# Optimization experiments

Hardware: AMD Instinct MI355X
Metric: run time of the kernel (lower is better)

Reference implementation:

```python
import jax, jax.numpy as jnp
import numpy as np

DIM = 384
NUM_HEADS = 12
WIN = (8, 8, 8)
Q_TOK = 1
K_TOK = 1
B = 64
N = WIN[0] * WIN[1] * WIN[2]  # 512


def _build_rel_index():
    t = max(Q_TOK, K_TOK)
    max_rel = [(w - 1) * t for w in WIN]
    nbins = [2 * m + 1 for m in max_rel]
    def coords(tok):
        axes = [np.arange(WIN[i]) * tok for i in range(3)]
        g = np.stack(np.meshgrid(*axes, indexing='ij'))  # [3, D, H, W]
        return g.reshape(3, -1)  # [3, N]
    cq = coords(Q_TOK)
    ck = coords(K_TOK)
    rel = (cq[:, :, None] - ck[:, None, :]).transpose(1, 2, 0)  # [N, N, 3]
    rel = rel + np.array(max_rel)
    idx = rel[..., 0] * (nbins[1] * nbins[2]) + rel[..., 1] * nbins[2] + rel[..., 2]
    return idx.astype(np.int32), nbins[0] * nbins[1] * nbins[2]


def setup_inputs() -> dict:
    key = jax.random.key(0)
    ks = jax.random.split(key, 7)
    rel_index_np, num_rel = _build_rel_index()
    s = 0.02
    return {
        'x1': jax.random.normal(ks[0], (B, N, DIM), jnp.float32),
        'x2': jax.random.normal(ks[1], (B, N, DIM), jnp.float32),
        'Wq': jax.random.normal(ks[2], (DIM, DIM), jnp.float32) * s,
        'Wkv': jax.random.normal(ks[3], (2 * DIM, DIM), jnp.float32) * s,
        'q_bias': jax.random.normal(ks[4], (DIM,), jnp.float32) * s,
        'v_bias': jax.random.normal(ks[5], (DIM,), jnp.float32) * s,
        'bias_table': jax.random.normal(ks[6], (num_rel, NUM_HEADS), jnp.float32) * s,
        'rel_index': jnp.asarray(rel_index_np),  # [N, N] int32
    }


def reference(x1, x2, Wq, Wkv, q_bias, v_bias, bias_table, rel_index):
    Bq, N1, C = x1.shape
    N2 = x2.shape[1]
    H = NUM_HEADS
    hd = C // H

    q = x1 @ Wq.T + q_bias                      # [B, N1, C]
    kv_bias = jnp.concatenate([jnp.zeros_like(v_bias), v_bias])
    kv = x2 @ Wkv.T + kv_bias                   # [B, N2, 2C]

    q = q.reshape(Bq, N1, H, hd).transpose(0, 2, 1, 3)   # [B, H, N1, hd]
    kv = kv.reshape(Bq, N2, 2, H, hd).transpose(2, 0, 3, 1, 4)
    k, v = kv[0], kv[1]                          # [B, H, N2, hd]

    # relative position bias: gather [N1, N2, H] -> [H, N1, N2]
    bias = bias_table[rel_index]                 # [N1, N2, H]
    bias = bias.transpose(2, 0, 1)               # [H, N1, N2]

    scale = 1.0 / jnp.sqrt(jnp.asarray(hd, q.dtype))
    scores = jnp.einsum('bhqd,bhkd->bhqk', q, k) * scale + bias[None]
    attn = jax.nn.softmax(scores, axis=-1)
    out = jnp.einsum('bhqk,bhkd->bhqd', attn, v)  # [B, H, N1, hd]
    return out.transpose(0, 2, 1, 3).reshape(Bq, N1, C)
```

## Files before the change

### kernel.cpp

```cpp
#include <hip/hip_runtime.h>

typedef unsigned short u16;
typedef unsigned int u32;
typedef __bf16 bf16x8 __attribute__((ext_vector_type(8)));
typedef float f32x4 __attribute__((ext_vector_type(4)));
typedef u16 u16x8 __attribute__((ext_vector_type(8)));
typedef u32 u32x4 __attribute__((ext_vector_type(4)));

#define NB 64
#define NN 512
#define NH 12
#define HD 32
#define DIM 384

static constexpr size_t QWS = (size_t)NB * NH * NN * HD;
#define LOG2E 1.4426950408889634f
#define QSCALE 0.25503486f

__device__ __forceinline__ u16 f2bf(float f) {
  __bf16 b = (__bf16)f;
  union { __bf16 b; u16 u; } v; v.b = b;
  return v.u;
}
__device__ __forceinline__ float lo16f(u32 w) {
  union { u32 u; float f; } v; v.u = w << 16;
  return v.f;
}
__device__ __forceinline__ float hi16f(u32 w) {
  union { u32 u; float f; } v; v.u = w & 0xffff0000u;
  return v.f;
}

__global__ __launch_bounds__(256) void bias_expand_k(const float* __restrict__ table,
                                                     const int* __restrict__ rel,
                                                     u32* __restrict__ beR) {
  int t = blockIdx.x * 256 + threadIdx.x;
  int word = t & 3;
  int lane = (t >> 2) & 63;
  int mf   = (t >> 8) & 3;
  int wv   = (t >> 10) & 7;
  int kt   = (t >> 13) & 15;
  int h    = t >> 17;
  int lr = lane & 15, lg = lane >> 4;
  int q = wv * 64 + mf * 16 + lr;
  int k = kt * 32 + (word >> 1) * 16 + lg * 4 + (word & 1) * 2;
  int i0 = rel[q * NN + k];
  int i1 = rel[q * NN + k + 1];
  u16 b0 = f2bf(table[i0 * NH + h] * LOG2E);
  u16 b1 = f2bf(table[i1 * NH + h] * LOG2E);
  beR[t] = (u32)b0 | ((u32)b1 << 16);
}

__global__ __launch_bounds__(256) void qkv_proj_k(const float* __restrict__ x1,
                                                  const float* __restrict__ x2,
                                                  const float* __restrict__ Wq,
                                                  const float* __restrict__ Wkv,
                                                  const float* __restrict__ qb,
                                                  const float* __restrict__ vb,
                                                  u16* __restrict__ q_ws,
                                                  u16* __restrict__ k_ws,
                                                  u16* __restrict__ v_ws) {
  const int g = blockIdx.x;
  const int v = (g & 7) * 288 + (g >> 3);
  const int ct = v % 9;
  const int m0 = (v / 9) * 128;
  const int j0 = ct * 128;
  const float* A;
  const float* W;
  int type;
  if (ct < 3)      { A = x1; W = Wq  + (size_t)j0 * DIM;         type = 0; }
  else if (ct < 6) { A = x2; W = Wkv + (size_t)(j0 - 384) * DIM; type = 1; }
  else             { A = x2; W = Wkv + (size_t)(j0 - 384) * DIM; type = 2; }

  __shared__ u16 As[128][72];
  __shared__ u16 Bs[128][72];

  const int tid = threadIdx.x;
  const int lane = tid & 63, wid = tid >> 6;
  const int wm = (wid >> 1) * 64, wn = (wid & 1) * 64;
  const int lg = lane >> 4, lr = lane & 15;
  const int srow = tid >> 3;
  const int scol = (tid & 7) * 8;

  f32x4 acc[4][4] = {};

  for (int k0 = 0; k0 < DIM; k0 += 64) {
    __syncthreads();
#pragma unroll
    for (int rr = 0; rr < 4; ++rr) {
      int r = srow + rr * 32;
      const float* src = A + (size_t)(m0 + r) * DIM + k0 + scol;
      float4 f0 = *(const float4*)src;
      float4 f1 = *(const float4*)(src + 4);
      u16x8 tmp = {f2bf(f0.x), f2bf(f0.y), f2bf(f0.z), f2bf(f0.w),
                   f2bf(f1.x), f2bf(f1.y), f2bf(f1.z), f2bf(f1.w)};
      *(u16x8*)&As[r][scol] = tmp;
      const float* srcB = W + (size_t)r * DIM + k0 + scol;
      float4 g0 = *(const float4*)srcB;
      float4 g1 = *(const float4*)(srcB + 4);
      u16x8 tmpB = {f2bf(g0.x), f2bf(g0.y), f2bf(g0.z), f2bf(g0.w),
                    f2bf(g1.x), f2bf(g1.y), f2bf(g1.z), f2bf(g1.w)};
      *(u16x8*)&Bs[r][scol] = tmpB;
    }
    __syncthreads();
#pragma unroll
    for (int kk = 0; kk < 2; ++kk) {
      bf16x8 af[4], bfv[4];
#pragma unroll
      for (int mf = 0; mf < 4; ++mf)
        af[mf] = *(const bf16x8*)&As[wm + mf * 16 + lr][kk * 32 + lg * 8];
#pragma unroll
      for (int nf = 0; nf < 4; ++nf)
        bfv[nf] = *(const bf16x8*)&Bs[wn + nf * 16 + lr][kk * 32 + lg * 8];
#pragma unroll
      for (int mf = 0; mf < 4; ++mf)
#pragma unroll
        for (int nf = 0; nf < 4; ++nf)
          acc[mf][nf] = __builtin_amdgcn_mfma_f32_16x16x32_bf16(af[mf], bfv[nf], acc[mf][nf], 0, 0, 0);
    }
  }

  const int b = m0 >> 9;
  u16* dst = (type == 0) ? q_ws : (type == 1 ? k_ws : v_ws);
  const float scale = (type == 0) ? QSCALE : 1.0f;
#pragma unroll
  for (int nf = 0; nf < 4; ++nf) {
    int j = j0 + wn + nf * 16 + lr;
    int jj = j - ((type == 0) ? 0 : (type == 1 ? 384 : 768));
    float bv = (type == 0) ? qb[jj] : (type == 2 ? vb[jj] : 0.0f);
    int h = jj >> 5, d = jj & 31;
    u16* dcol = dst + (((size_t)b * NH + h) * NN) * HD + d;
#pragma unroll
    for (int mf = 0; mf < 4; ++mf) {
      int nbase = (m0 & 511) + wm + mf * 16 + lg * 4;
#pragma unroll
      for (int r = 0; r < 4; ++r) {
        float val = (acc[mf][nf][r] + bv) * scale;
        dcol[(size_t)(nbase + r) * HD] = f2bf(val);
      }
    }
  }
}

__global__ __launch_bounds__(512, 4) void attn_k(const u16* __restrict__ qw,
                                                 const u16* __restrict__ kw,
                                                 const u16* __restrict__ vw,
                                                 const u32* __restrict__ beR,
                                                 float* __restrict__ out) {
  const int g = blockIdx.x;
  const int vv = (g & 7) * 96 + (g >> 3);
  const int h = vv >> 6, b = vv & 63;
  const size_t base = ((size_t)b * NH + h) * NN * HD;
  const u16* Q = qw + base;
  const u16* K = kw + base;
  const u16* V = vw + base;

  __shared__ u16 Ks[NN][40];
  __shared__ u16 Vtp[HD][520];

  const int tid = threadIdx.x;
  const int lane = tid & 63, w = tid >> 6;
  const int lg = lane >> 4, lr = lane & 15;
  const int q0 = w * 64;

  bf16x8 qf[4];
#pragma unroll
  for (int mf = 0; mf < 4; ++mf)
    qf[mf] = *(const bf16x8*)&Q[(q0 + mf * 16 + lr) * HD + lg * 8];

  for (int c = tid; c < 2048; c += 512) {
    int row = c >> 2, part = (c & 3) * 8;
    *(u16x8*)&Ks[row][part] = *(const u16x8*)&K[row * HD + part];
    u16x8 vld = *(const u16x8*)&V[row * HD + part];
    int kk = row & 31;
    int col = (row & ~31) + ((kk >> 2) & 3) * 8 + (kk >> 4) * 4 + (kk & 3);
#pragma unroll
    for (int j = 0; j < 8; ++j) Vtp[part + j][col] = vld[j];
  }
  __syncthreads();

  const u32* bstream = beR + ((((size_t)h * 16) * 8 + w) * 4) * 256 + lane * 4;

  f32x4 accOT[4][2] = {};
  float lsum[4] = {0.f, 0.f, 0.f, 0.f};

  for (int kt = 0; kt < 16; ++kt) {
    const int k0 = kt * 32;
    const u32* bkt = bstream + (size_t)kt * 8192;
    bf16x8 kf0 = *(const bf16x8*)&Ks[k0 + lr][lg * 8];
    bf16x8 kf1 = *(const bf16x8*)&Ks[k0 + 16 + lr][lg * 8];
    bf16x8 vp0 = *(const bf16x8*)&Vtp[lr][k0 + lg * 8];
    bf16x8 vp1 = *(const bf16x8*)&Vtp[16 + lr][k0 + lg * 8];
#pragma unroll
    for (int mf = 0; mf < 4; ++mf) {
      u32x4 bb = *(const u32x4*)(bkt + mf * 256);
      f32x4 c0 = {lo16f(bb.x), hi16f(bb.x), lo16f(bb.y), hi16f(bb.y)};
      f32x4 c1 = {lo16f(bb.z), hi16f(bb.z), lo16f(bb.w), hi16f(bb.w)};
      f32x4 s0 = __builtin_amdgcn_mfma_f32_16x16x32_bf16(kf0, qf[mf], c0, 0, 0, 0);
      f32x4 s1 = __builtin_amdgcn_mfma_f32_16x16x32_bf16(kf1, qf[mf], c1, 0, 0, 0);
      float p0[4], p1[4];
#pragma unroll
      for (int r = 0; r < 4; ++r) {
        p0[r] = __builtin_amdgcn_exp2f(s0[r]);
        p1[r] = __builtin_amdgcn_exp2f(s1[r]);
      }
      lsum[mf] += ((p0[0] + p0[1]) + (p0[2] + p0[3])) +
                  ((p1[0] + p1[1]) + (p1[2] + p1[3]));
      bf16x8 pv = {(__bf16)p0[0], (__bf16)p0[1], (__bf16)p0[2], (__bf16)p0[3],
                   (__bf16)p1[0], (__bf16)p1[1], (__bf16)p1[2], (__bf16)p1[3]};
      accOT[mf][0] = __builtin_amdgcn_mfma_f32_16x16x32_bf16(vp0, pv, accOT[mf][0], 0, 0, 0);
      accOT[mf][1] = __builtin_amdgcn_mfma_f32_16x16x32_bf16(vp1, pv, accOT[mf][1], 0, 0, 0);
    }
  }

  float linv[4];
#pragma unroll
  for (int mf = 0; mf < 4; ++mf) {
    float s = lsum[mf];
    s += __shfl_xor(s, 16, 64);
    s += __shfl_xor(s, 32, 64);
    linv[mf] = 1.0f / s;
  }

  float* outp = out + ((size_t)b * NN) * DIM + h * HD;
#pragma unroll
  for (int mf = 0; mf < 4; ++mf) {
    int q = q0 + mf * 16 + lr;
#pragma unroll
    for (int nf = 0; nf < 2; ++nf) {
      float4 o = {accOT[mf][nf][0] * linv[mf], accOT[mf][nf][1] * linv[mf],
                  accOT[mf][nf][2] * linv[mf], accOT[mf][nf][3] * linv[mf]};
      *(float4*)&outp[(size_t)q * DIM + nf * 16 + lg * 4] = o;
    }
  }
}

extern "C" void kernel_launch(void* const* d_in, const int* in_sizes, int n_in,
                              void* d_out, int out_size, void* d_ws, size_t ws_size,
                              hipStream_t stream) {
  const float* x1    = (const float*)d_in[0];
  const float* x2    = (const float*)d_in[1];
  const float* Wq    = (const float*)d_in[2];
  const float* Wkv   = (const float*)d_in[3];
  const float* qb    = (const float*)d_in[4];
  const float* vb    = (const float*)d_in[5];
  const float* table = (const float*)d_in[6];
  const int*   rel   = (const int*)d_in[7];
  float* out = (float*)d_out;

  u16* ws   = (u16*)d_ws;
  u16* q_ws = ws;
  u16* k_ws = ws + QWS;
  u16* v_ws = ws + 2 * QWS;
  u32* beR  = (u32*)(ws + 3 * QWS);

  bias_expand_k<<<6144, 256, 0, stream>>>(table, rel, beR);
  qkv_proj_k<<<2304, 256, 0, stream>>>(x1, x2, Wq, Wkv, qb, vb, q_ws, k_ws, v_ws);
  attn_k<<<NB * NH, 512, 0, stream>>>(q_ws, k_ws, v_ws, beR, out);
}
```

Before: 120.3 us.

## Pre-convert weights to bf16 fragment layout and stream them via LDS DMA

Folds the weight fp32-to-bf16 conversion into the bias-expansion prep kernel, writing weights into a fragment-ordered bf16 buffer. The QKV projection is restructured so each 512-thread block holds a 128-row strip of activations in registers for the full K=384 and streams weight chunks through double-buffered LDS using global_load_lds. This removes the repeated per-tile reconversion of weights and of activations across column tiles, at the cost of many more registers per thread, fewer and larger blocks, and strided 2-byte output stores.

```diff
diff --git a/kernel.cpp b/kernel.cpp
--- a/kernel.cpp
+++ b/kernel.cpp
@@ -30,115 +30,120 @@
   union { u32 u; float f; } v; v.u = w & 0xffff0000u;
   return v.f;
 }
-
-__global__ __launch_bounds__(256) void bias_expand_k(const float* __restrict__ table,
-                                                     const int* __restrict__ rel,
-                                                     u32* __restrict__ beR) {
-  int t = blockIdx.x * 256 + threadIdx.x;
-  int word = t & 3;
-  int lane = (t >> 2) & 63;
-  int mf   = (t >> 8) & 3;
-  int wv   = (t >> 10) & 7;
-  int kt   = (t >> 13) & 15;
-  int h    = t >> 17;
-  int lr = lane & 15, lg = lane >> 4;
-  int q = wv * 64 + mf * 16 + lr;
-  int k = kt * 32 + (word >> 1) * 16 + lg * 4 + (word & 1) * 2;
-  int i0 = rel[q * NN + k];
-  int i1 = rel[q * NN + k + 1];
-  u16 b0 = f2bf(table[i0 * NH + h] * LOG2E);
-  u16 b1 = f2bf(table[i1 * NH + h] * LOG2E);
-  beR[t] = (u32)b0 | ((u32)b1 << 16);
-}
-
-__global__ __launch_bounds__(256) void qkv_proj_k(const float* __restrict__ x1,
-                                                  const float* __restrict__ x2,
-                                                  const float* __restrict__ Wq,
-                                                  const float* __restrict__ Wkv,
-                                                  const float* __restrict__ qb,
-                                                  const float* __restrict__ vb,
-                                                  u16* __restrict__ q_ws,
-                                                  u16* __restrict__ k_ws,
-                                                  u16* __restrict__ v_ws) {
-  const int g = blockIdx.x;
-  const int v = (g & 7) * 288 + (g >> 3);
-  const int ct = v % 9;
-  const int m0 = (v / 9) * 128;
-  const int j0 = ct * 128;
-  const float* A;
-  const float* W;
-  int type;
-  if (ct < 3)      { A = x1; W = Wq  + (size_t)j0 * DIM;         type = 0; }
-  else if (ct < 6) { A = x2; W = Wkv + (size_t)(j0 - 384) * DIM; type = 1; }
-  else             { A = x2; W = Wkv + (size_t)(j0 - 384) * DIM; type = 2; }
-
-  __shared__ u16 As[128][72];
-  __shared__ u16 Bs[128][72];
-
-  const int tid = threadIdx.x;
-  const int lane = tid & 63, wid = tid >> 6;
-  const int wm = (wid >> 1) * 64, wn = (wid & 1) * 64;
+__device__ __forceinline__ void gload16(const void* g, void* l) {
+  __builtin_amdgcn_global_load_lds((const __attribute__((address_space(1))) u32*)g,
+                                   (__attribute__((address_space(3))) u32*)l, 16, 0, 0);
+}
+
+__global__ __launch_bounds__(256) void prep_k(const float* __restrict__ table,
+                                              const int* __restrict__ rel,
+                                              const float* __restrict__ Wq,
+                                              const float* __restrict__ Wkv,
+                                              u32* __restrict__ beR,
+                                              u16* __restrict__ Wf) {
+  int bid = blockIdx.x;
+  if (bid < 6144) {
+    int t = bid * 256 + threadIdx.x;
+    int word = t & 3;
+    int lane = (t >> 2) & 63;
+    int mf   = (t >> 8) & 3;
+    int wv   = (t >> 10) & 7;
+    int kt   = (t >> 13) & 15;
+    int h    = t >> 17;
+    int lr = lane & 15, lg = lane >> 4;
+    int q = wv * 64 + mf * 16 + lr;
+    int k = kt * 32 + (word >> 1) * 16 + lg * 4 + (word & 1) * 2;
+    int i0 = rel[q * NN + k];
+    int i1 = rel[q * NN + k + 1];
+    u16 b0 = f2bf(table[i0 * NH + h] * LOG2E);
+    u16 b1 = f2bf(table[i1 * NH + h] * LOG2E);
+    beR[t] = (u32)b0 | ((u32)b1 << 16);
+  } else {
+    int t2 = (bid - 6144) * 256 + threadIdx.x;
+    int lane = t2 & 63;
+    int kk = (t2 >> 6) % 12;
+    int cb = t2 / (12 * 64);
+    int j = cb * 16 + (lane & 15);
+    int k = kk * 32 + (lane >> 4) * 8;
+    const float* wrow = (j < 384) ? (Wq + (size_t)j * DIM) : (Wkv + (size_t)(j - 384) * DIM);
+    float4 a = *(const float4*)(wrow + k);
+    float4 b = *(const float4*)(wrow + k + 4);
+    u16x8 o = {f2bf(a.x), f2bf(a.y), f2bf(a.z), f2bf(a.w),
+               f2bf(b.x), f2bf(b.y), f2bf(b.z), f2bf(b.w)};
+    *(u16x8*)(Wf + (size_t)t2 * 8) = o;
+  }
+}
+
+__global__ __launch_bounds__(512, 4) void qkv_proj_k(const float* __restrict__ x1,
+                                                     const float* __restrict__ x2,
+                                                     const float* __restrict__ qb,
+                                                     const float* __restrict__ vb,
+                                                     const u16* __restrict__ Wf,
+                                                     u16* __restrict__ q_ws,
+                                                     u16* __restrict__ k_ws,
+                                                     u16* __restrict__ v_ws) {
+  __shared__ __attribute__((aligned(16))) u16 Wbuf[2][12288];
+
+  const int bid = blockIdx.x;
+  const int is_q = bid >= 256;
+  const int m0 = (bid & 255) * 128;
+  const int tid = threadIdx.x, lane = tid & 63, w = tid >> 6;
   const int lg = lane >> 4, lr = lane & 15;
-  const int srow = tid >> 3;
-  const int scol = (tid & 7) * 8;
-
-  f32x4 acc[4][4] = {};
-
-  for (int k0 = 0; k0 < DIM; k0 += 64) {
+  const float* X = is_q ? x1 : x2;
+  const int cb0 = is_q ? 0 : 24;
+  const int nch = is_q ? 12 : 24;
+  const char* wsrc = (const char*)(Wf + (size_t)cb0 * 12 * 64 * 8);
+  const int bb = m0 >> 9;
+
+  bf16x8 af[12];
+  const float* xrow = X + (size_t)(m0 + w * 16 + lr) * DIM + lg * 8;
+#pragma unroll
+  for (int kk = 0; kk < 12; ++kk) {
+    float4 a = *(const float4*)(xrow + kk * 32);
+    float4 b = *(const float4*)(xrow + kk * 32 + 4);
+    af[kk] = (bf16x8){(__bf16)a.x, (__bf16)a.y, (__bf16)a.z, (__bf16)a.w,
+                      (__bf16)b.x, (__bf16)b.y, (__bf16)b.z, (__bf16)b.w};
+  }
+
+#pragma unroll
+  for (int i = 0; i < 3; ++i) {
+    int inst = w + i * 8;
+    gload16(wsrc + inst * 1024 + lane * 16, (char*)&Wbuf[0][0] + inst * 1024 + lane * 16);
+  }
+  __syncthreads();
+
+  for (int c = 0; c < nch; ++c) {
+    if (c + 1 < nch) {
+      const char* s = wsrc + (size_t)(c + 1) * 24576;
+      char* d = (char*)&Wbuf[(c + 1) & 1][0];
+#pragma unroll
+      for (int i = 0; i < 3; ++i) {
+        int inst = w + i * 8;
+        gload16(s + inst * 1024 + lane * 16, d + inst * 1024 + lane * 16);
+      }
+    }
+    const u16* wb = &Wbuf[c & 1][0];
+#pragma unroll
+    for (int lc = 0; lc < 2; ++lc) {
+      f32x4 acc = {0.f, 0.f, 0.f, 0.f};
+#pragma unroll
+      for (int kk = 0; kk < 12; ++kk) {
+        bf16x8 wf = *(const bf16x8*)(wb + ((lc * 12 + kk) * 64 + lane) * 8);
+        acc = __builtin_amdgcn_mfma_f32_16x16x32_bf16(af[kk], wf, acc, 0, 0, 0);
+      }
+      int j = (cb0 + c * 2 + lc) * 16 + lr;
+      int jj = is_q ? j : (j < 768 ? j - 384 : j - 768);
+      float bv = is_q ? qb[jj] : (j >= 768 ? vb[jj] : 0.0f);
+      float scale = is_q ? QSCALE : 1.0f;
+      u16* dst = is_q ? q_ws : (j < 768 ? k_ws : v_ws);
+      int hh = jj >> 5, dd = jj & 31;
+      size_t basead = ((size_t)(bb * NH + hh) * NN) * HD + dd;
+      int rowb = (m0 & 511) + w * 16 + lg * 4;
+#pragma unroll
+      for (int r = 0; r < 4; ++r)
+        dst[basead + (size_t)(rowb + r) * HD] = f2bf((acc[r] + bv) * scale);
+    }
     __syncthreads();
-#pragma unroll
-    for (int rr = 0; rr < 4; ++rr) {
-      int r = srow + rr * 32;
-      const float* src = A + (size_t)(m0 + r) * DIM + k0 + scol;
-      float4 f0 = *(const float4*)src;
-      float4 f1 = *(const float4*)(src + 4);
-      u16x8 tmp = {f2bf(f0.x), f2bf(f0.y), f2bf(f0.z), f2bf(f0.w),
-                   f2bf(f1.x), f2bf(f1.y), f2bf(f1.z), f2bf(f1.w)};
-      *(u16x8*)&As[r][scol] = tmp;
-      const float* srcB = W + (size_t)r * DIM + k0 + scol;
-      float4 g0 = *(const float4*)srcB;
-      float4 g1 = *(const float4*)(srcB + 4);
-      u16x8 tmpB = {f2bf(g0.x), f2bf(g0.y), f2bf(g0.z), f2bf(g0.w),
-                    f2bf(g1.x), f2bf(g1.y), f2bf(g1.z), f2bf(g1.w)};
-      *(u16x8*)&Bs[r][scol] = tmpB;
-    }
-    __syncthreads();
-#pragma unroll
-    for (int kk = 0; kk < 2; ++kk) {
-      bf16x8 af[4], bfv[4];
-#pragma unroll
-      for (int mf = 0; mf < 4; ++mf)
-        af[mf] = *(const bf16x8*)&As[wm + mf * 16 + lr][kk * 32 + lg * 8];
-#pragma unroll
-      for (int nf = 0; nf < 4; ++nf)
-        bfv[nf] = *(const bf16x8*)&Bs[wn + nf * 16 + lr][kk * 32 + lg * 8];
-#pragma unroll
-      for (int mf = 0; mf < 4; ++mf)
-#pragma unroll
-        for (int nf = 0; nf < 4; ++nf)
-          acc[mf][nf] = __builtin_amdgcn_mfma_f32_16x16x32_bf16(af[mf], bfv[nf], acc[mf][nf], 0, 0, 0);
-    }
-  }
-
-  const int b = m0 >> 9;
-  u16* dst = (type == 0) ? q_ws : (type == 1 ? k_ws : v_ws);
-  const float scale = (type == 0) ? QSCALE : 1.0f;
-#pragma unroll
-  for (int nf = 0; nf < 4; ++nf) {
-    int j = j0 + wn + nf * 16 + lr;
-    int jj = j - ((type == 0) ? 0 : (type == 1 ? 384 : 768));
-    float bv = (type == 0) ? qb[jj] : (type == 2 ? vb[jj] : 0.0f);
-    int h = jj >> 5, d = jj & 31;
-    u16* dcol = dst + (((size_t)b * NH + h) * NN) * HD + d;
-#pragma unroll
-    for (int mf = 0; mf < 4; ++mf) {
-      int nbase = (m0 & 511) + wm + mf * 16 + lg * 4;
-#pragma unroll
-      for (int r = 0; r < 4; ++r) {
-        float val = (acc[mf][nf][r] + bv) * scale;
-        dcol[(size_t)(nbase + r) * HD] = f2bf(val);
-      }
-    }
   }
 }
 
@@ -193,9 +198,9 @@
     bf16x8 vp1 = *(const bf16x8*)&Vtp[16 + lr][k0 + lg * 8];
 #pragma unroll
     for (int mf = 0; mf < 4; ++mf) {
-      u32x4 bb = *(const u32x4*)(bkt + mf * 256);
-      f32x4 c0 = {lo16f(bb.x), hi16f(bb.x), lo16f(bb.y), hi16f(bb.y)};
-      f32x4 c1 = {lo16f(bb.z), hi16f(bb.z), lo16f(bb.w), hi16f(bb.w)};
+      u32x4 bbv = *(const u32x4*)(bkt + mf * 256);
+      f32x4 c0 = {lo16f(bbv.x), hi16f(bbv.x), lo16f(bbv.y), hi16f(bbv.y)};
+      f32x4 c1 = {lo16f(bbv.z), hi16f(bbv.z), lo16f(bbv.w), hi16f(bbv.w)};
       f32x4 s0 = __builtin_amdgcn_mfma_f32_16x16x32_bf16(kf0, qf[mf], c0, 0, 0, 0);
       f32x4 s1 = __builtin_amdgcn_mfma_f32_16x16x32_bf16(kf1, qf[mf], c1, 0, 0, 0);
       float p0[4], p1[4];
@@ -253,8 +258,9 @@
   u16* k_ws = ws + QWS;
   u16* v_ws = ws + 2 * QWS;
   u32* beR  = (u32*)(ws + 3 * QWS);
-
-  bias_expand_k<<<6144, 256, 0, stream>>>(table, rel, beR);
-  qkv_proj_k<<<2304, 256, 0, stream>>>(x1, x2, Wq, Wkv, qb, vb, q_ws, k_ws, v_ws);
+  u16* Wf   = ws + 3 * QWS + 2 * 1572864;
+
+  prep_k<<<6360, 256, 0, stream>>>(table, rel, Wq, Wkv, beR, Wf);
+  qkv_proj_k<<<512, 512, 0, stream>>>(x1, x2, qb, vb, Wf, q_ws, k_ws, v_ws);
   attn_k<<<NB * NH, 512, 0, stream>>>(q_ws, k_ws, v_ws, beR, out);
 }
```

Measured after the change: 107.1 us. 10.9% less time.
